# Performance work log

Hardware: AMD Instinct MI355X
Metric: run time of the kernel (lower is better)

## Reference

```python
import jax, jax.numpy as jnp
import numpy as np

HIDDEN = 1024
HEAD = 64
B, T = 4, 4096

def setup_inputs() -> dict:
    key = jax.random.key(0)
    kx, kq, kk, kv = jax.random.split(key, 4)
    bound = 1.0 / np.sqrt(HIDDEN)  # nn.Linear default init range
    x = jax.random.normal(kx, (B, T, HIDDEN), dtype=jnp.float32)
    W_Q = jax.random.uniform(kq, (HIDDEN, HEAD), jnp.float32, -bound, bound)
    W_K = jax.random.uniform(kk, (HIDDEN, HEAD), jnp.float32, -bound, bound)
    W_V = jax.random.uniform(kv, (HIDDEN, HEAD), jnp.float32, -bound, bound)
    return {"x": x, "W_Q": W_Q, "W_K": W_K, "W_V": W_V}

def reference(x, W_Q, W_K, W_V):
    # Q,K,V: [B,T,HEAD]
    Q = x @ W_Q
    K = x @ W_K
    V = x @ W_V
    scale = 1.0 / np.sqrt(HEAD).astype(np.float32)
    scores = jnp.einsum('bqd,bkd->bqk', Q, K) * scale  # [B,T,T]
    Tlen = x.shape[1]
    causal = jnp.tril(jnp.ones((Tlen, Tlen), dtype=bool))
    scores = jnp.where(causal, scores, -jnp.inf)
    attn = jax.nn.softmax(scores, axis=-1)
    # dropout=0.0 -> identity
    return jnp.einsum('bqk,bkd->bqd', attn, V)
```

## Files before the change

kernel.cpp:

```cpp
#include <hip/hip_runtime.h>

typedef short bf16x8 __attribute__((ext_vector_type(8)));
typedef float f32x4 __attribute__((ext_vector_type(4)));

#define T_LEN 4096
#define NB    4
#define HID   1024
#define HD    64

__device__ __forceinline__ unsigned short f2bf(float f) {
    union { float f; unsigned int u; } v; v.f = f;
    unsigned int u = v.u;
    u += 0x7fffu + ((u >> 16) & 1u);
    return (unsigned short)(u >> 16);
}

__device__ __forceinline__ void gl_lds16(const float* g, float* l) {
    __builtin_amdgcn_global_load_lds(
        (const __attribute__((address_space(1))) unsigned int*)g,
        (__attribute__((address_space(3))) unsigned int*)l, 16, 0, 0);
}

__global__ __launch_bounds__(256) void wtrans_kernel(
    const float* __restrict__ wq, const float* __restrict__ wk,
    const float* __restrict__ wv, unsigned short* __restrict__ Wpk)
{
    const int idx = blockIdx.x * 256 + threadIdx.x;
    const int k = idx & 1023;
    const int n = idx >> 10;
    const float* w = (n < 64) ? wq : ((n < 128) ? wk : wv);
    const int ks = k >> 5, g = (k >> 3) & 3, j = k & 7;
    const int nt = n >> 4, lr = n & 15;
    const int lane = g * 16 + lr;
    Wpk[((size_t)(ks * 12 + nt) << 9) + (lane << 3) + j] =
        f2bf(w[(size_t)k * 64 + (n & 63)]);
}

__global__ __launch_bounds__(256, 4) void qkv_proj_kernel(
    const float* __restrict__ x, const unsigned short* __restrict__ Wpk,
    unsigned short* __restrict__ Qb, unsigned short* __restrict__ Kpk,
    unsigned short* __restrict__ Vpk)
{
    __shared__ __align__(16) float xs[2][2048];
    const int tid = threadIdx.x;
    const int w = tid >> 6, lane = tid & 63;
    const int g = lane >> 4, lr = lane & 15;
    const int t0 = blockIdx.x * 16;

    const int r0 = (w << 2) + (lane >> 5);
    const int r1 = r0 + 2;
    const int pc = lane & 31;
    const float* gs0 = x + (size_t)(t0 + r0) * HID + ((pc ^ (r0 & 7)) << 2);
    const float* gs1 = x + (size_t)(t0 + r1) * HID + ((pc ^ (r1 & 7)) << 2);
    const int lb0 = w << 9;
    const int lb1 = lb0 + 256;

    f32x4 acc[3];
#pragma unroll
    for (int i = 0; i < 3; ++i) acc[i] = (f32x4)(0.0f);

    gl_lds16(gs0, &xs[0][lb0]);
    gl_lds16(gs1, &xs[0][lb1]);
    __syncthreads();

    for (int t = 0; t < 8; ++t) {
        const int cur = t & 1;
        if (t < 7) {
            gl_lds16(gs0 + (t + 1) * 128, &xs[cur ^ 1][lb0]);
            gl_lds16(gs1 + (t + 1) * 128, &xs[cur ^ 1][lb1]);
        }
#pragma unroll
        for (int kk = 0; kk < 4; ++kk) {
            const int lc0 = kk * 8 + g * 2;
            const float4 a0 = *(const float4*)&xs[cur][lr * 128 + ((lc0 ^ (lr & 7)) << 2)];
            const float4 a1 = *(const float4*)&xs[cur][lr * 128 + (((lc0 + 1) ^ (lr & 7)) << 2)];
            bf16x8 af;
            af[0] = (short)f2bf(a0.x); af[1] = (short)f2bf(a0.y);
            af[2] = (short)f2bf(a0.z); af[3] = (short)f2bf(a0.w);
            af[4] = (short)f2bf(a1.x); af[5] = (short)f2bf(a1.y);
            af[6] = (short)f2bf(a1.z); af[7] = (short)f2bf(a1.w);
            const unsigned short* wp =
                Wpk + (((size_t)((t * 4 + kk) * 12 + w * 3)) << 9) + (lane << 3);
#pragma unroll
            for (int j = 0; j < 3; ++j) {
                const bf16x8 bfr = *(const bf16x8*)(wp + ((size_t)j << 9));
                acc[j] = __builtin_amdgcn_mfma_f32_16x16x32_bf16(af, bfr, acc[j], 0, 0, 0);
            }
        }
        __syncthreads();
    }

    const size_t bpk = (size_t)(t0 >> 12) * (T_LEN * HD);
#pragma unroll
    for (int j = 0; j < 3; ++j) {
        const int nt = w * 3 + j;
#pragma unroll
        for (int r = 0; r < 4; ++r) {
            const int grow = t0 + g * 4 + r;
            const unsigned short val = f2bf(acc[j][r]);
            if (nt < 4) {
                Qb[(size_t)grow * HD + nt * 16 + lr] = val;
            } else if (nt < 8) {
                const int tl = grow & 4095, d = (nt - 4) * 16 + lr;
                Kpk[bpk + ((((tl >> 4) * 8 + (d >> 3)) * 16 + (tl & 15)) << 3) + (d & 7)] = val;
            } else {
                const int tl = grow & 4095, d = (nt - 8) * 16 + lr;
                Vpk[bpk + (((tl >> 3) * 64 + d) << 3) + (tl & 7)] = val;
            }
        }
    }
}

#define MOFF 96.0f

__device__ __forceinline__ void kv_pair(
    const int t0, const int lane, const int g, const int lr,
    const unsigned short* __restrict__ kpk_b, const unsigned short* __restrict__ vpk_b,
    unsigned short (*P)[136],
    const bf16x8 qf0, const bf16x8 qf1,
    f32x4 oacc[4], float lrow[4])
{
    const float SCL = 0.18033688011112042f;
    f32x4 s[8];
    const unsigned short* kbase = kpk_b + (((size_t)(t0 >> 4)) << 10) + (lane << 3);
#pragma unroll
    for (int nt = 0; nt < 8; ++nt) {
        const bf16x8 kf0 = *(const bf16x8*)(kbase + ((size_t)nt << 10));
        const bf16x8 kf1 = *(const bf16x8*)(kbase + ((size_t)nt << 10) + 512);
        f32x4 a = (f32x4)(0.0f);
        a = __builtin_amdgcn_mfma_f32_16x16x32_bf16(qf0, kf0, a, 0, 0, 0);
        a = __builtin_amdgcn_mfma_f32_16x16x32_bf16(qf1, kf1, a, 0, 0, 0);
        s[nt] = a;
    }
#pragma unroll
    for (int nt = 0; nt < 8; ++nt)
#pragma unroll
        for (int r = 0; r < 4; ++r) {
            const float p = __builtin_amdgcn_exp2f((s[nt][r] - MOFF) * SCL);
            lrow[r] += p;
            P[g * 4 + r][nt * 16 + lr] = f2bf(p);
        }

    const bf16x8 pf0 = *(const bf16x8*)&P[lr][g * 8];
    const bf16x8 pf1 = *(const bf16x8*)&P[lr][32 + g * 8];
    const bf16x8 pf2 = *(const bf16x8*)&P[lr][64 + g * 8];
    const bf16x8 pf3 = *(const bf16x8*)&P[lr][96 + g * 8];
    const unsigned short* vb = vpk_b + (((size_t)((t0 >> 3) + g)) << 9) + (lr << 3);
#pragma unroll
    for (int dt = 0; dt < 4; ++dt) {
        const bf16x8 vf0 = *(const bf16x8*)(vb + dt * 128);
        const bf16x8 vf1 = *(const bf16x8*)(vb + (4 << 9) + dt * 128);
        const bf16x8 vf2 = *(const bf16x8*)(vb + (8 << 9) + dt * 128);
        const bf16x8 vf3 = *(const bf16x8*)(vb + (12 << 9) + dt * 128);
        oacc[dt] = __builtin_amdgcn_mfma_f32_16x16x32_bf16(pf0, vf0, oacc[dt], 0, 0, 0);
        oacc[dt] = __builtin_amdgcn_mfma_f32_16x16x32_bf16(pf1, vf1, oacc[dt], 0, 0, 0);
        oacc[dt] = __builtin_amdgcn_mfma_f32_16x16x32_bf16(pf2, vf2, oacc[dt], 0, 0, 0);
        oacc[dt] = __builtin_amdgcn_mfma_f32_16x16x32_bf16(pf3, vf3, oacc[dt], 0, 0, 0);
    }
}

template <bool MASKED>
__device__ __forceinline__ void kv_single(
    const int t0, const int qw0, const int lane, const int g, const int lr,
    const unsigned short* __restrict__ kpk_b, const unsigned short* __restrict__ vpk_b,
    unsigned short (*P)[136],
    const bf16x8 qf0, const bf16x8 qf1,
    f32x4 oacc[4], float lrow[4])
{
    const float SCL = 0.18033688011112042f;
    f32x4 s[4];
    const unsigned short* kbase = kpk_b + (((size_t)(t0 >> 4)) << 10) + (lane << 3);
#pragma unroll
    for (int nt = 0; nt < 4; ++nt) {
        const bf16x8 kf0 = *(const bf16x8*)(kbase + ((size_t)nt << 10));
        const bf16x8 kf1 = *(const bf16x8*)(kbase + ((size_t)nt << 10) + 512);
        f32x4 a = (f32x4)(0.0f);
        a = __builtin_amdgcn_mfma_f32_16x16x32_bf16(qf0, kf0, a, 0, 0, 0);
        a = __builtin_amdgcn_mfma_f32_16x16x32_bf16(qf1, kf1, a, 0, 0, 0);
        s[nt] = a;
    }
    if (MASKED) {
#pragma unroll
        for (int nt = 0; nt < 4; ++nt) {
            const int kj = t0 + nt * 16 + lr;
#pragma unroll
            for (int r = 0; r < 4; ++r)
                if (kj > qw0 + g * 4 + r) s[nt][r] = -3.0e38f;
        }
    }
#pragma unroll
    for (int nt = 0; nt < 4; ++nt)
#pragma unroll
        for (int r = 0; r < 4; ++r) {
            const float p = __builtin_amdgcn_exp2f((s[nt][r] - MOFF) * SCL);
            lrow[r] += p;
            P[g * 4 + r][nt * 16 + lr] = f2bf(p);
        }

    const bf16x8 pf0 = *(const bf16x8*)&P[lr][g * 8];
    const bf16x8 pf1 = *(const bf16x8*)&P[lr][32 + g * 8];
    const unsigned short* vb = vpk_b + (((size_t)((t0 >> 3) + g)) << 9) + (lr << 3);
#pragma unroll
    for (int dt = 0; dt < 4; ++dt) {
        const bf16x8 vf0 = *(const bf16x8*)(vb + dt * 128);
        const bf16x8 vf1 = *(const bf16x8*)(vb + (4 << 9) + dt * 128);
        oacc[dt] = __builtin_amdgcn_mfma_f32_16x16x32_bf16(pf0, vf0, oacc[dt], 0, 0, 0);
        oacc[dt] = __builtin_amdgcn_mfma_f32_16x16x32_bf16(pf1, vf1, oacc[dt], 0, 0, 0);
    }
}

__global__ __launch_bounds__(64) void attn_part_kernel(
    const unsigned short* __restrict__ Qb, const unsigned short* __restrict__ Kpk,
    const unsigned short* __restrict__ Vpk,
    float* __restrict__ Opart, float* __restrict__ Lpart)
{
    int i = blockIdx.x;
    const int b = i / 1152;
    i -= b * 1152;
    int c = 0, rem = i;
#pragma unroll
    for (int cc = 0; cc < 8; ++cc) {
        const int cnt = 256 - (cc << 5);
        if (c == cc && rem >= cnt) { rem -= cnt; c = cc + 1; }
    }
    const int qt = (c << 5) + rem;

    __shared__ unsigned short Plds[16][136];
    const int lane = threadIdx.x & 63;
    const int g = lane >> 4, lr = lane & 15;
    const int qw0 = qt << 4;
    const int kvbase = c << 9;

    const unsigned short* qp = Qb + (size_t)((b << 12) + qw0 + lr) * HD + g * 8;
    const bf16x8 qf0 = *(const bf16x8*)qp;
    const bf16x8 qf1 = *(const bf16x8*)(qp + 32);
    const unsigned short* kpk_b = Kpk + (size_t)b * (T_LEN * HD);
    const unsigned short* vpk_b = Vpk + (size_t)b * (T_LEN * HD);

    f32x4 oacc[4];
#pragma unroll
    for (int i2 = 0; i2 < 4; ++i2) oacc[i2] = (f32x4)(0.0f);
    float lrow[4] = {0.f, 0.f, 0.f, 0.f};

    const bool diag = ((qt >> 5) == c);
    const int nfull = diag ? ((qw0 - kvbase + 1) >> 6) : 8;
    int it = 0;
    for (; it + 2 <= nfull; it += 2)
        kv_pair(kvbase + it * 64, lane, g, lr, kpk_b, vpk_b, Plds, qf0, qf1, oacc, lrow);
    if (it < nfull)
        kv_single<false>(kvbase + it * 64, qw0, lane, g, lr, kpk_b, vpk_b, Plds,
                         qf0, qf1, oacc, lrow);
    if (diag)
        kv_single<true>(kvbase + nfull * 64, qw0, lane, g, lr, kpk_b, vpk_b, Plds,
                        qf0, qf1, oacc, lrow);

#pragma unroll
    for (int m = 1; m < 16; m <<= 1)
#pragma unroll
        for (int r = 0; r < 4; ++r) lrow[r] += __shfl_xor(lrow[r], m, 64);

    const size_t p = ((size_t)((b << 8) + qt) << 3) + c;
    float* Op = Opart + (p << 10);
    float* Lp = Lpart + (p << 4);
#pragma unroll
    for (int r = 0; r < 4; ++r) {
        const int wrow = g * 4 + r;
        if (lr == 0) Lp[wrow] = lrow[r];
#pragma unroll
        for (int dt = 0; dt < 4; ++dt)
            Op[wrow * 64 + dt * 16 + lr] = oacc[dt][r];
    }
}

__global__ __launch_bounds__(256) void attn_merge_kernel(
    const float* __restrict__ Opart, const float* __restrict__ Lpart,
    float* __restrict__ out)
{
    const int qt = blockIdx.x & 255, b = blockIdx.x >> 8;
    const int nch = (qt >> 5) + 1;
    const int t = threadIdx.x;
    const int row = t >> 4, d0 = (t & 15) << 2;
    const size_t pb = (size_t)blockIdx.x << 3;

    float L = 0.f;
#pragma unroll
    for (int c = 0; c < 8; ++c)
        if (c < nch) L += Lpart[((pb + c) << 4) + row];
    const float inv = 1.0f / L;

    f32x4 o = (f32x4)(0.0f);
#pragma unroll
    for (int c = 0; c < 8; ++c) {
        if (c < nch) {
            const f32x4 v = *(const f32x4*)(Opart + (((pb + c) << 4) + row) * 64 + d0);
#pragma unroll
            for (int j = 0; j < 4; ++j) o[j] += v[j];
        }
    }
    f32x4 res;
#pragma unroll
    for (int j = 0; j < 4; ++j) res[j] = o[j] * inv;
    *(f32x4*)(out + (size_t)((b << 12) + (qt << 4) + row) * HD + d0) = res;
}

extern "C" void kernel_launch(void* const* d_in, const int* in_sizes, int n_in,
                              void* d_out, int out_size, void* d_ws, size_t ws_size,
                              hipStream_t stream) {
    const float* x  = (const float*)d_in[0];
    const float* wq = (const float*)d_in[1];
    const float* wk = (const float*)d_in[2];
    const float* wv = (const float*)d_in[3];
    float* out = (float*)d_out;

    float* Opart = (float*)d_ws;
    float* Lpart = Opart + ((size_t)8192 * 1024);
    unsigned short* Qb  = (unsigned short*)(Lpart + (size_t)8192 * 16);
    unsigned short* Kpk = Qb  + (size_t)NB * T_LEN * HD;
    unsigned short* Vpk = Kpk + (size_t)NB * T_LEN * HD;
    unsigned short* Wpk = Vpk + (size_t)NB * T_LEN * HD;

    wtrans_kernel<<<768, 256, 0, stream>>>(wq, wk, wv, Wpk);
    qkv_proj_kernel<<<1024, 256, 0, stream>>>(x, Wpk, Qb, Kpk, Vpk);
    attn_part_kernel<<<NB * 1152, 64, 0, stream>>>(Qb, Kpk, Vpk, Opart, Lpart);
    attn_merge_kernel<<<NB * 256, 256, 0, stream>>>(Opart, Lpart, out);
}
```

Before: 66.74 us.

## Restructure projection to single-wave blocks and group four query tiles per attention block

The QKV projection now runs one wave per block that computes all 12 output column tiles. It relies on explicit vmcnt waits instead of block barriers, which removes __syncthreads but gives each wave four times the MFMA and weight-load work and fewer waves per block. The attention partial kernel packs four 16-row query tiles into one 256-thread block with per-wave P buffers, so it launches fewer, larger blocks. The merge kernel is reshaped to handle 64 rows per block to match the new partial layout.

Measured after the change: 145.0 us. 117% more time.

```diff
diff --git a/kernel.cpp b/kernel.cpp
--- a/kernel.cpp
+++ b/kernel.cpp
@@ -20,6 +20,8 @@
         (const __attribute__((address_space(1))) unsigned int*)g,
         (__attribute__((address_space(3))) unsigned int*)l, 16, 0, 0);
 }
+
+#define VMCNT_WAIT(n) asm volatile("s_waitcnt vmcnt(" #n ")" ::: "memory")
 
 __global__ __launch_bounds__(256) void wtrans_kernel(
     const float* __restrict__ wq, const float* __restrict__ wk,
@@ -36,38 +38,41 @@
         f2bf(w[(size_t)k * 64 + (n & 63)]);
 }
 
-__global__ __launch_bounds__(256, 4) void qkv_proj_kernel(
+__global__ void qkv_proj_kernel(
     const float* __restrict__ x, const unsigned short* __restrict__ Wpk,
     unsigned short* __restrict__ Qb, unsigned short* __restrict__ Kpk,
     unsigned short* __restrict__ Vpk)
 {
     __shared__ __align__(16) float xs[2][2048];
-    const int tid = threadIdx.x;
-    const int w = tid >> 6, lane = tid & 63;
+    const int lane = threadIdx.x & 63;
     const int g = lane >> 4, lr = lane & 15;
     const int t0 = blockIdx.x * 16;
-
-    const int r0 = (w << 2) + (lane >> 5);
-    const int r1 = r0 + 2;
+    const int h = lane >> 5;
     const int pc = lane & 31;
-    const float* gs0 = x + (size_t)(t0 + r0) * HID + ((pc ^ (r0 & 7)) << 2);
-    const float* gs1 = x + (size_t)(t0 + r1) * HID + ((pc ^ (r1 & 7)) << 2);
-    const int lb0 = w << 9;
-    const int lb1 = lb0 + 256;
-
-    f32x4 acc[3];
-#pragma unroll
-    for (int i = 0; i < 3; ++i) acc[i] = (f32x4)(0.0f);
-
-    gl_lds16(gs0, &xs[0][lb0]);
-    gl_lds16(gs1, &xs[0][lb1]);
-    __syncthreads();
+
+    const float* srcs[8];
+#pragma unroll
+    for (int i = 0; i < 8; ++i) {
+        const int rl = 2 * i + h;
+        srcs[i] = x + (size_t)(t0 + rl) * HID + ((pc ^ (rl & 7)) << 2);
+    }
+
+    f32x4 acc[12];
+#pragma unroll
+    for (int i = 0; i < 12; ++i) acc[i] = (f32x4)(0.0f);
+
+#pragma unroll
+    for (int i = 0; i < 8; ++i) gl_lds16(srcs[i], &xs[0][i * 256]);
 
     for (int t = 0; t < 8; ++t) {
         const int cur = t & 1;
         if (t < 7) {
-            gl_lds16(gs0 + (t + 1) * 128, &xs[cur ^ 1][lb0]);
-            gl_lds16(gs1 + (t + 1) * 128, &xs[cur ^ 1][lb1]);
+#pragma unroll
+            for (int i = 0; i < 8; ++i)
+                gl_lds16(srcs[i] + (t + 1) * 128, &xs[cur ^ 1][i * 256]);
+            VMCNT_WAIT(8);
+        } else {
+            VMCNT_WAIT(0);
         }
 #pragma unroll
         for (int kk = 0; kk < 4; ++kk) {
@@ -80,24 +85,22 @@
             af[4] = (short)f2bf(a1.x); af[5] = (short)f2bf(a1.y);
             af[6] = (short)f2bf(a1.z); af[7] = (short)f2bf(a1.w);
             const unsigned short* wp =
-                Wpk + (((size_t)((t * 4 + kk) * 12 + w * 3)) << 9) + (lane << 3);
-#pragma unroll
-            for (int j = 0; j < 3; ++j) {
+                Wpk + (((size_t)((t * 4 + kk) * 12)) << 9) + (lane << 3);
+#pragma unroll
+            for (int j = 0; j < 12; ++j) {
                 const bf16x8 bfr = *(const bf16x8*)(wp + ((size_t)j << 9));
                 acc[j] = __builtin_amdgcn_mfma_f32_16x16x32_bf16(af, bfr, acc[j], 0, 0, 0);
             }
         }
-        __syncthreads();
     }
 
     const size_t bpk = (size_t)(t0 >> 12) * (T_LEN * HD);
 #pragma unroll
-    for (int j = 0; j < 3; ++j) {
-        const int nt = w * 3 + j;
+    for (int nt = 0; nt < 12; ++nt) {
 #pragma unroll
         for (int r = 0; r < 4; ++r) {
             const int grow = t0 + g * 4 + r;
-            const unsigned short val = f2bf(acc[j][r]);
+            const unsigned short val = f2bf(acc[nt][r]);
             if (nt < 4) {
                 Qb[(size_t)grow * HD + nt * 16 + lr] = val;
             } else if (nt < 8) {
@@ -209,27 +212,29 @@
     }
 }
 
-__global__ __launch_bounds__(64) void attn_part_kernel(
+__global__ __launch_bounds__(256) void attn_part_kernel(
     const unsigned short* __restrict__ Qb, const unsigned short* __restrict__ Kpk,
     const unsigned short* __restrict__ Vpk,
     float* __restrict__ Opart, float* __restrict__ Lpart)
 {
     int i = blockIdx.x;
-    const int b = i / 1152;
-    i -= b * 1152;
+    const int b = i / 288;
+    i -= b * 288;
     int c = 0, rem = i;
 #pragma unroll
     for (int cc = 0; cc < 8; ++cc) {
-        const int cnt = 256 - (cc << 5);
+        const int cnt = 64 - (cc << 3);
         if (c == cc && rem >= cnt) { rem -= cnt; c = cc + 1; }
     }
-    const int qt = (c << 5) + rem;
-
-    __shared__ unsigned short Plds[16][136];
-    const int lane = threadIdx.x & 63;
+    const int qb = (c << 3) + rem;
+
+    __shared__ unsigned short Plds[4][16][136];
+    const int tid = threadIdx.x;
+    const int wave = tid >> 6, lane = tid & 63;
     const int g = lane >> 4, lr = lane & 15;
-    const int qw0 = qt << 4;
+    const int qw0 = (qb << 6) + (wave << 4);
     const int kvbase = c << 9;
+    unsigned short (*P)[136] = Plds[wave];
 
     const unsigned short* qp = Qb + (size_t)((b << 12) + qw0 + lr) * HD + g * 8;
     const bf16x8 qf0 = *(const bf16x8*)qp;
@@ -242,16 +247,16 @@
     for (int i2 = 0; i2 < 4; ++i2) oacc[i2] = (f32x4)(0.0f);
     float lrow[4] = {0.f, 0.f, 0.f, 0.f};
 
-    const bool diag = ((qt >> 5) == c);
+    const bool diag = ((qb >> 3) == c);
     const int nfull = diag ? ((qw0 - kvbase + 1) >> 6) : 8;
     int it = 0;
     for (; it + 2 <= nfull; it += 2)
-        kv_pair(kvbase + it * 64, lane, g, lr, kpk_b, vpk_b, Plds, qf0, qf1, oacc, lrow);
+        kv_pair(kvbase + it * 64, lane, g, lr, kpk_b, vpk_b, P, qf0, qf1, oacc, lrow);
     if (it < nfull)
-        kv_single<false>(kvbase + it * 64, qw0, lane, g, lr, kpk_b, vpk_b, Plds,
+        kv_single<false>(kvbase + it * 64, qw0, lane, g, lr, kpk_b, vpk_b, P,
                          qf0, qf1, oacc, lrow);
     if (diag)
-        kv_single<true>(kvbase + nfull * 64, qw0, lane, g, lr, kpk_b, vpk_b, Plds,
+        kv_single<true>(kvbase + nfull * 64, qw0, lane, g, lr, kpk_b, vpk_b, P,
                         qf0, qf1, oacc, lrow);
 
 #pragma unroll
@@ -259,12 +264,12 @@
 #pragma unroll
         for (int r = 0; r < 4; ++r) lrow[r] += __shfl_xor(lrow[r], m, 64);
 
-    const size_t p = ((size_t)((b << 8) + qt) << 3) + c;
-    float* Op = Opart + (p << 10);
-    float* Lp = Lpart + (p << 4);
+    const size_t p = ((size_t)((b << 6) + qb) << 3) + c;
+    float* Op = Opart + (p << 12);
+    float* Lp = Lpart + (p << 6);
 #pragma unroll
     for (int r = 0; r < 4; ++r) {
-        const int wrow = g * 4 + r;
+        const int wrow = (wave << 4) + g * 4 + r;
         if (lr == 0) Lp[wrow] = lrow[r];
 #pragma unroll
         for (int dt = 0; dt < 4; ++dt)
@@ -276,31 +281,41 @@
     const float* __restrict__ Opart, const float* __restrict__ Lpart,
     float* __restrict__ out)
 {
-    const int qt = blockIdx.x & 255, b = blockIdx.x >> 8;
-    const int nch = (qt >> 5) + 1;
+    const int qb = blockIdx.x & 63, b = blockIdx.x >> 6;
+    const int nch = (qb >> 3) + 1;
     const int t = threadIdx.x;
-    const int row = t >> 4, d0 = (t & 15) << 2;
+    const int row = t >> 2, d0 = (t & 3) << 4;
     const size_t pb = (size_t)blockIdx.x << 3;
 
     float L = 0.f;
 #pragma unroll
     for (int c = 0; c < 8; ++c)
-        if (c < nch) L += Lpart[((pb + c) << 4) + row];
+        if (c < nch) L += Lpart[((pb + c) << 6) + row];
     const float inv = 1.0f / L;
 
-    f32x4 o = (f32x4)(0.0f);
+    f32x4 o[4];
+#pragma unroll
+    for (int i = 0; i < 4; ++i) o[i] = (f32x4)(0.0f);
 #pragma unroll
     for (int c = 0; c < 8; ++c) {
         if (c < nch) {
-            const f32x4 v = *(const f32x4*)(Opart + (((pb + c) << 4) + row) * 64 + d0);
-#pragma unroll
-            for (int j = 0; j < 4; ++j) o[j] += v[j];
-        }
-    }
-    f32x4 res;
-#pragma unroll
-    for (int j = 0; j < 4; ++j) res[j] = o[j] * inv;
-    *(f32x4*)(out + (size_t)((b << 12) + (qt << 4) + row) * HD + d0) = res;
+            const f32x4* src = (const f32x4*)(Opart + (((pb + c) << 12) + row * 64 + d0));
+#pragma unroll
+            for (int i = 0; i < 4; ++i) {
+                const f32x4 v = src[i];
+#pragma unroll
+                for (int j = 0; j < 4; ++j) o[i][j] += v[j];
+            }
+        }
+    }
+    f32x4* dst = (f32x4*)(out + (size_t)((b << 12) + (qb << 6) + row) * HD + d0);
+#pragma unroll
+    for (int i = 0; i < 4; ++i) {
+        f32x4 res;
+#pragma unroll
+        for (int j = 0; j < 4; ++j) res[j] = o[i][j] * inv;
+        dst[i] = res;
+    }
 }
 
 extern "C" void kernel_launch(void* const* d_in, const int* in_sizes, int n_in,
@@ -313,14 +328,14 @@
     float* out = (float*)d_out;
 
     float* Opart = (float*)d_ws;
-    float* Lpart = Opart + ((size_t)8192 * 1024);
-    unsigned short* Qb  = (unsigned short*)(Lpart + (size_t)8192 * 16);
+    float* Lpart = Opart + ((size_t)2048 * 4096);
+    unsigned short* Qb  = (unsigned short*)(Lpart + (size_t)2048 * 64);
     unsigned short* Kpk = Qb  + (size_t)NB * T_LEN * HD;
     unsigned short* Vpk = Kpk + (size_t)NB * T_LEN * HD;
     unsigned short* Wpk = Vpk + (size_t)NB * T_LEN * HD;
 
     wtrans_kernel<<<768, 256, 0, stream>>>(wq, wk, wv, Wpk);
-    qkv_proj_kernel<<<1024, 256, 0, stream>>>(x, Wpk, Qb, Kpk, Vpk);
-    attn_part_kernel<<<NB * 1152, 64, 0, stream>>>(Qb, Kpk, Vpk, Opart, Lpart);
-    attn_merge_kernel<<<NB * 256, 256, 0, stream>>>(Opart, Lpart, out);
-}
+    qkv_proj_kernel<<<1024, 64, 0, stream>>>(x, Wpk, Qb, Kpk, Vpk);
+    attn_part_kernel<<<NB * 288, 256, 0, stream>>>(Qb, Kpk, Vpk, Opart, Lpart);
+    attn_merge_kernel<<<NB * 64, 256, 0, stream>>>(Opart, Lpart, out);
+}
```
